# Optimization experiments

Hardware: AMD Instinct MI355X
Metric: run time of the kernel (lower is better)

## Reference

```python
import jax, jax.numpy as jnp
import numpy as np

EPS = 1e-5


def tbn(x, g, b):
    # TensorBatchNorm2d(121): normalize each of the 11x11 tensor entries over (B, C, H, W)
    mu = x.mean(axis=(0, 1, 2, 3), keepdims=True)
    var = ((x - mu) ** 2).mean(axis=(0, 1, 2, 3), keepdims=True)
    return (x - mu) * jax.lax.rsqrt(var + EPS) * g + b


def prelu(x, a):
    return jnp.where(x >= 0, x, a * x)


def tconv1x1(x, U, V):
    # x: [B,1,H,W,m,n]; U: [p,m]; V: [q,n] -> y[...,p,q] = U @ X @ V^T
    return jnp.einsum('bchwmn,pm,qn->bchwpq', x, U, V)


def tconv3x3(x, U, V):
    # x: [B,1,H,W,m,n]; U,V: [3,3,p,m] / [3,3,q,n]; pad=1, stride=1
    H, W = x.shape[2], x.shape[3]
    xp = jnp.pad(x, ((0, 0), (0, 0), (1, 1), (1, 1), (0, 0), (0, 0)))
    y = jnp.zeros(x.shape[:4] + (U.shape[2], V.shape[2]), x.dtype)
    for i in range(3):
        for j in range(3):
            y = y + jnp.einsum('bchwmn,pm,qn->bchwpq', xp[:, :, i:i + H, j:j + W], U[i, j], V[i, j])
    return y


def forward(x, f0_U, f0_V, f0_g, f0_b, f0_a, s_U, s_V, s_g, s_b,
            blk_U1, blk_V1, blk_g1, blk_b1, blk_a1,
            blk_U2, blk_V2, blk_g2, blk_b2, blk_a2,
            blk_U3, blk_V3, blk_g3, blk_b3, head_W):
    # view(-1,8,16,16,32,32).permute(0,1,4,5,2,3) -> [B,8,32,32,16,16]
    x = x.reshape(-1, 8, 16, 16, 32, 32).transpose(0, 1, 4, 5, 2, 3)
    B, H, W = x.shape[0], 32, 32
    # f0: 3x3 tensorized conv, 8 channels -> 1, tensor 16x16 -> 11x11
    xp = jnp.pad(x, ((0, 0), (0, 0), (1, 1), (1, 1), (0, 0), (0, 0)))
    y = jnp.zeros((B, H, W, 11, 11), x.dtype)
    for i in range(3):
        for j in range(3):
            y = y + jnp.einsum('bchwmn,cpm,cqn->bhwpq', xp[:, :, i:i + H, j:j + W], f0_U[:, i, j], f0_V[:, i, j])
    h = prelu(tbn(y[:, None], f0_g, f0_b), f0_a)  # [B,1,32,32,11,11]
    for k in range(4):  # four residual bottleneck blocks with 1x1 shortcut
        idn = tbn(tconv1x1(h, s_U[k], s_V[k]), s_g[k], s_b[k])
        z = prelu(tbn(tconv1x1(h, blk_U1[k], blk_V1[k]), blk_g1[k], blk_b1[k]), blk_a1[k])
        z = prelu(tbn(tconv3x3(z, blk_U2[k], blk_V2[k]), blk_g2[k], blk_b2[k]), blk_a2[k])
        z = tbn(tconv1x1(z, blk_U3[k], blk_V3[k]), blk_g3[k], blk_b3[k])
        h = z + idn
    # fcn_head: 1x1, out_type=0 -> fully contract the [11,11] tensor per class
    return jnp.einsum('bchwmn,omn->bohw', h, head_W)  # [B,21,32,32]


def setup_inputs():
    ks = jax.random.split(jax.random.key(0), 26)
    r = lambda i, s: jax.random.normal(ks[i], s, dtype=jnp.float32)
    return {
        'x': r(0, (64, 8, 16, 16, 32, 32)),
        'f0_U': r(1, (8, 3, 3, 11, 16)) * 0.1,
        'f0_V': r(2, (8, 3, 3, 11, 16)) * 0.1,
        'f0_g': r(3, (11, 11)), 'f0_b': r(4, (11, 11)),
        'f0_a': jnp.float32(0.25),
        's_U': r(5, (4, 11, 11)) * 0.3, 's_V': r(6, (4, 11, 11)) * 0.3,
        's_g': r(7, (4, 11, 11)), 's_b': r(8, (4, 11, 11)),
        'blk_U1': r(9, (4, 11, 11)) * 0.3, 'blk_V1': r(10, (4, 11, 11)) * 0.3,
        'blk_g1': r(11, (4, 11, 11)), 'blk_b1': r(12, (4, 11, 11)),
        'blk_a1': jax.random.uniform(ks[13], (4,), dtype=jnp.float32),
        'blk_U2': r(14, (4, 3, 3, 11, 11)) * 0.2, 'blk_V2': r(15, (4, 3, 3, 11, 11)) * 0.2,
        'blk_g2': r(16, (4, 11, 11)), 'blk_b2': r(17, (4, 11, 11)),
        'blk_a2': jax.random.uniform(ks[18], (4,), dtype=jnp.float32),
        'blk_U3': r(19, (4, 11, 11)) * 0.3, 'blk_V3': r(20, (4, 11, 11)) * 0.3,
        'blk_g3': r(21, (4, 11, 11)), 'blk_b3': r(22, (4, 11, 11)),
        'head_W': r(23, (21, 11, 11)) * 0.1,
    }


def reference(x, f0_U, f0_V, f0_g, f0_b, f0_a, s_U, s_V, s_g, s_b,
              blk_U1, blk_V1, blk_g1, blk_b1, blk_a1,
              blk_U2, blk_V2, blk_g2, blk_b2, blk_a2,
              blk_U3, blk_V3, blk_g3, blk_b3, head_W):
    return forward(x, f0_U, f0_V, f0_g, f0_b, f0_a, s_U, s_V, s_g, s_b,
                   blk_U1, blk_V1, blk_g1, blk_b1, blk_a1,
                   blk_U2, blk_V2, blk_g2, blk_b2, blk_a2,
                   blk_U3, blk_V3, blk_g3, blk_b3, head_W)
```

## Files before the change

### kernel.cpp

```cpp
#include <hip/hip_runtime.h>

#define NPOS 65536
#define NE   121
#define NP   6
#define NPP  4

__device__ __forceinline__ void gload_lds16(const float* g, float* l) {
  __builtin_amdgcn_global_load_lds(
      (const __attribute__((address_space(1))) void*)g,
      (__attribute__((address_space(3))) void*)l, 16, 0, 0);
}

__device__ __forceinline__ void fin_from_part(int e, const float* __restrict__ pp,
                                              const float* __restrict__ g,
                                              const float* __restrict__ bb,
                                              float& sc, float& sh) {
  float s  = pp[e * 4] + pp[e * 4 + 1] + pp[e * 4 + 2] + pp[e * 4 + 3];
  float s2 = pp[484 + e * 4] + pp[484 + e * 4 + 1] +
             pp[484 + e * 4 + 2] + pp[484 + e * 4 + 3];
  float mu  = s  * (1.f / 65536.f);
  float var = s2 * (1.f / 65536.f) - mu * mu;
  sc = g[e] * rsqrtf(var + 1e-5f);
  sh = bb[e] - mu * sc;
}

__global__ __launch_bounds__(256, 1)
void f0_kernel(const float* __restrict__ x, const float* __restrict__ U,
               const float* __restrict__ V, float* __restrict__ y,
               float* __restrict__ psum, float* __restrict__ psq) {
  __shared__ float Xb[16384];
  __shared__ float su[1152];
  __shared__ float sv[1728];

  int bid = blockIdx.x;
  int wg  = (bid & 7) * 512 + (bid >> 3);
  int ph  = wg & 1;
  int row = wg >> 1;
  int b = row >> 5, h = row & 31;
  int P0 = ph * 5;
  int t = threadIdx.x;
  int s = t >> 5, w = t & 31;

  int hlo = (h == 0) ? 0 : h - 1;
  int hhi = (h == 31) ? 31 : h + 1;
  int nh = hhi - hlo + 1;
  int nslab = 8 * nh;

  float Y[NP][11];
#pragma unroll
  for (int p = 0; p < NP; ++p)
#pragma unroll
    for (int q = 0; q < 11; ++q) Y[p][q] = 0.f;

  auto stageUV = [&](int c) {
    for (int idx = t; idx < 1152; idx += 256) {
      int tap = idx >> 7, r = idx & 127;
      int m = r >> 3, pr = r & 7;
      su[idx] = (pr < 6) ? U[(c * 9 + tap) * 176 + (P0 + pr) * 16 + m] : 0.f;
    }
    for (int idx = t; idx < 1728; idx += 256) {
      int tap = idx / 192, r = idx - tap * 192;
      int n = r / 12, q = r - n * 12;
      sv[idx] = (q < 11) ? V[(c * 9 + tap) * 176 + q * 16 + n] : 0.f;
    }
  };

  auto issueX = [&](int k) {
    int c = k / nh, hi = hlo + k % nh;
    const float* base = x + ((size_t)(b * 8 + c) << 18) + hi * 32;
    float* buf = &Xb[(k & 1) * 8192];
    int wv = t >> 6, ln = t & 63;
#pragma unroll
    for (int kk = 0; kk < 8; ++kk) {
      int chunk = wv * 8 + kk;
      int mn = chunk * 8 + (ln >> 3);
      gload_lds16(base + (size_t)mn * 1024 + (ln & 7) * 4, buf + chunk * 256);
    }
  };

  stageUV(0);
  issueX(0);

  for (int k = 0; k < nslab; ++k) {
    asm volatile("s_waitcnt vmcnt(0)" ::: "memory");
    __syncthreads();
    if (k + 1 < nslab) issueX(k + 1);

    const float* Xt = &Xb[(k & 1) * 8192];
    int c = k / nh, hi = hlo + k % nh;
    int tapbase = (hi - h + 1) * 3;
#pragma unroll
    for (int j = 0; j < 3; ++j) {
      int wj = w + j - 1;
      if ((unsigned)wj < 32u) {
        int tap = tapbase + j;
        const float* suT = &su[tap * 128];
        const float* svT = &sv[tap * 192];
        float A0[6], A1[6];
#pragma unroll
        for (int p = 0; p < 6; ++p) { A0[p] = 0.f; A1[p] = 0.f; }
#pragma unroll
        for (int m = 0; m < 16; ++m) {
          float x0 = Xt[(m * 16 + 2 * s) * 32 + wj];
          float x1 = Xt[(m * 16 + 2 * s + 1) * 32 + wj];
          float4 u0 = *(const float4*)&suT[m * 8];
          float2 u1 = *(const float2*)&suT[m * 8 + 4];
          A0[0] += u0.x * x0; A1[0] += u0.x * x1;
          A0[1] += u0.y * x0; A1[1] += u0.y * x1;
          A0[2] += u0.z * x0; A1[2] += u0.z * x1;
          A0[3] += u0.w * x0; A1[3] += u0.w * x1;
          A0[4] += u1.x * x0; A1[4] += u1.x * x1;
          A0[5] += u1.y * x0; A1[5] += u1.y * x1;
        }
#pragma unroll
        for (int nn = 0; nn < 2; ++nn) {
          const float* vb = &svT[(2 * s + nn) * 12];
          float4 v0 = *(const float4*)&vb[0];
          float4 v1 = *(const float4*)&vb[4];
          float4 v2 = *(const float4*)&vb[8];
          float vq[11] = { v0.x, v0.y, v0.z, v0.w,
                           v1.x, v1.y, v1.z, v1.w,
                           v2.x, v2.y, v2.z };
          const float* Ax = nn ? A1 : A0;
#pragma unroll
          for (int p = 0; p < 6; ++p)
#pragma unroll
            for (int q = 0; q < 11; ++q)
              Y[p][q] += Ax[p] * vq[q];
        }
      }
    }
    if (k + 1 < nslab && (k % nh) == nh - 1) {
      __syncthreads();
      stageUV(c + 1);
    }
  }

  int posb = ((b << 5) + h) << 5;
#pragma unroll
  for (int p = 0; p < NP; ++p) {
    __syncthreads();
#pragma unroll
    for (int q = 0; q < 11; ++q) Xb[t * 11 + q] = Y[p][q];
    __syncthreads();
    for (int rep = 0; rep < 2; ++rep) {
      int idx = rep * 256 + t;
      if (idx < 352) {
        int qq = idx >> 5, w2 = idx & 31;
        float v = 0.f;
#pragma unroll
        for (int s2 = 0; s2 < 8; ++s2) v += Xb[(s2 * 32 + w2) * 11 + qq];
        int e = (P0 + p) * 11 + qq;
        y[(size_t)e * NPOS + posb + w2] = v;
        float sm = v, sq = v * v;
#pragma unroll
        for (int d = 16; d > 0; d >>= 1) {
          sm += __shfl_down(sm, d, 32);
          sq += __shfl_down(sq, d, 32);
        }
        if (w2 == 0) {
          psum[(size_t)e * 2048 + row] = sm;
          psq [(size_t)e * 2048 + row] = sq;
        }
      }
    }
  }
}

__global__ __launch_bounds__(256)
void f0_stats_final(const float* __restrict__ psum, const float* __restrict__ psq,
                    const float* __restrict__ g, const float* __restrict__ bb,
                    float* __restrict__ sc, float* __restrict__ sh) {
  int e = blockIdx.x, t = threadIdx.x;
  float s = 0.f, s2 = 0.f;
  for (int i = t; i < 2048; i += 256) {
    s  += psum[(size_t)e * 2048 + i];
    s2 += psq [(size_t)e * 2048 + i];
  }
#pragma unroll
  for (int o = 32; o > 0; o >>= 1) {
    s  += __shfl_down(s, o);
    s2 += __shfl_down(s2, o);
  }
  __shared__ float ls[8];
  int wid = t >> 6;
  if ((t & 63) == 0) { ls[wid] = s; ls[4 + wid] = s2; }
  __syncthreads();
  if (t == 0) {
    float ss  = ls[0] + ls[1] + ls[2] + ls[3];
    float ss2 = ls[4] + ls[5] + ls[6] + ls[7];
    float mu  = ss  * (1.f / 65536.f);
    float var = ss2 * (1.f / 65536.f) - mu * mu;
    float sca = g[e] * rsqrtf(var + 1e-5f);
    sc[e] = sca;
    sh[e] = bb[e] - mu * sca;
  }
}

__global__ __launch_bounds__(256)
void stats_partial(const float* __restrict__ raw, float* __restrict__ part) {
  int blk = blockIdx.x;
  int e = blk >> 2, qt = blk & 3;
  const float4* p = (const float4*)(raw + (size_t)e * NPOS) + qt * 4096;
  int t = threadIdx.x;
  float s = 0.f, s2 = 0.f;
  for (int i = t; i < 4096; i += 256) {
    float4 v = p[i];
    s  += v.x + v.y + v.z + v.w;
    s2 += v.x * v.x + v.y * v.y + v.z * v.z + v.w * v.w;
  }
#pragma unroll
  for (int o = 32; o > 0; o >>= 1) {
    s  += __shfl_down(s, o);
    s2 += __shfl_down(s2, o);
  }
  __shared__ float ls[8];
  int wid = t >> 6;
  if ((t & 63) == 0) { ls[wid] = s; ls[4 + wid] = s2; }
  __syncthreads();
  if (t == 0) {
    part[blk]       = ls[0] + ls[1] + ls[2] + ls[3];
    part[484 + blk] = ls[4] + ls[5] + ls[6] + ls[7];
  }
}

__global__ __launch_bounds__(256)
void stats_partial_dual(const float* __restrict__ rawA, float* __restrict__ partA,
                        const float* __restrict__ rawB, float* __restrict__ partB) {
  int blk = blockIdx.x;
  int sel = blk >= 484;
  int lblk = sel ? blk - 484 : blk;
  const float* raw = sel ? rawB : rawA;
  float* part = sel ? partB : partA;
  int e = lblk >> 2, qt = lblk & 3;
  const float4* p = (const float4*)(raw + (size_t)e * NPOS) + qt * 4096;
  int t = threadIdx.x;
  float s = 0.f, s2 = 0.f;
  for (int i = t; i < 4096; i += 256) {
    float4 v = p[i];
    s  += v.x + v.y + v.z + v.w;
    s2 += v.x * v.x + v.y * v.y + v.z * v.z + v.w * v.w;
  }
#pragma unroll
  for (int o = 32; o > 0; o >>= 1) {
    s  += __shfl_down(s, o);
    s2 += __shfl_down(s2, o);
  }
  __shared__ float ls[8];
  int wid = t >> 6;
  if ((t & 63) == 0) { ls[wid] = s; ls[4 + wid] = s2; }
  __syncthreads();
  if (t == 0) {
    part[lblk]       = ls[0] + ls[1] + ls[2] + ls[3];
    part[484 + lblk] = ls[4] + ls[5] + ls[6] + ls[7];
  }
}

template<bool HASB, bool PRELU, bool FINA, bool FINB>
__global__ __launch_bounds__(256, 2)
void conv1x1_dual(const float* __restrict__ rA,
                  const float* __restrict__ scA, const float* __restrict__ shA,
                  const float* __restrict__ pA, const float* __restrict__ gA,
                  const float* __restrict__ bA,
                  const float* __restrict__ rB,
                  const float* __restrict__ pB, const float* __restrict__ gB,
                  const float* __restrict__ bB,
                  const float* __restrict__ alpha_ptr, int alpha_idx,
                  const float* __restrict__ U1, const float* __restrict__ V1,
                  float* __restrict__ out1,
                  const float* __restrict__ U2, const float* __restrict__ V2,
                  float* __restrict__ out2) {
  __shared__ float su1[NPP * 11], su2[NPP * 11], sv1[121], sv2[121];
  __shared__ float sa[242], sb[242];
  int bid = blockIdx.x;
  int wg  = (bid & 7) * 96 + (bid >> 3);
  int part = wg % 3, posblk = wg / 3;
  int P0 = part * 4;
  int pmax = (part == 2) ? 3 : 4;
  int t = threadIdx.x;
  if (t < 121) {
    sv1[t] = V1[t]; sv2[t] = V2[t];
    if (FINA) fin_from_part(t, pA, gA, bA, sa[t], sb[t]);
    else      { sa[t] = scA[t]; sb[t] = shA[t]; }
    if (HASB) {
      if (FINB) fin_from_part(t, pB, gB, bB, sa[121 + t], sb[121 + t]);
    }
  }
  if (t < NPP * 11) {
    int pr = t / 11, mm = t - pr * 11;
    int srow = P0 + pr; if (srow > 10) srow = 10;
    su1[t] = U1[srow * 11 + mm];
    su2[t] = U2[srow * 11 + mm];
  }
  __syncthreads();
  float alpha = 0.f;
  if (PRELU) alpha = alpha_ptr[alpha_idx];
  size_t pos = (size_t)posblk * 256 + t;

  float T1[NPP][11], T2[NPP][11];
#pragma unroll
  for (int p = 0; p < NPP; ++p)
#pragma unroll
    for (int n = 0; n < 11; ++n) { T1[p][n] = 0.f; T2[p][n] = 0.f; }

#pragma unroll 2
  for (int m = 0; m < 11; ++m) {
    float Xr[11];
#pragma unroll
    for (int n = 0; n < 11; ++n) {
      int e = m * 11 + n;
      float v = sa[e] * rA[(size_t)e * NPOS + pos] + sb[e];
      if (HASB) v += sa[121 + e] * rB[(size_t)e * NPOS + pos] + sb[121 + e];
      if (PRELU) v = v >= 0.f ? v : alpha * v;
      Xr[n] = v;
    }
#pragma unroll
    for (int p = 0; p < NPP; ++p) {
      float u1 = su1[p * 11 + m];
      float u2 = su2[p * 11 + m];
#pragma unroll
      for (int n = 0; n < 11; ++n) {
        T1[p][n] += u1 * Xr[n];
        T2[p][n] += u2 * Xr[n];
      }
    }
  }
#pragma unroll
  for (int q = 0; q < 11; ++q) {
    float Yc1[NPP], Yc2[NPP];
#pragma unroll
    for (int p = 0; p < NPP; ++p) { Yc1[p] = 0.f; Yc2[p] = 0.f; }
#pragma unroll
    for (int n = 0; n < 11; ++n) {
      float v1 = sv1[q * 11 + n];
      float v2 = sv2[q * 11 + n];
#pragma unroll
      for (int p = 0; p < NPP; ++p) {
        Yc1[p] += T1[p][n] * v1;
        Yc2[p] += T2[p][n] * v2;
      }
    }
    for (int p = 0; p < pmax; ++p) {
      out1[(size_t)((P0 + p) * 11 + q) * NPOS + pos] = Yc1[p];
      out2[(size_t)((P0 + p) * 11 + q) * NPOS + pos] = Yc2[p];
    }
  }
}

template<bool PRELU>
__global__ __launch_bounds__(256, 2)
void conv1x1_kernel(const float* __restrict__ rA,
                    const float* __restrict__ pA, const float* __restrict__ gA,
                    const float* __restrict__ bA,
                    const float* __restrict__ alpha_ptr, int alpha_idx,
                    const float* __restrict__ U, const float* __restrict__ V,
                    float* __restrict__ out) {
  __shared__ float su[NP * 11], sv[121], sa[242], sb[242];
  int bid = blockIdx.x;
  int wg  = (bid & 7) * 64 + (bid >> 3);
  int ph = wg & 1, posblk = wg >> 1;
  int P0 = ph * 5;
  int t = threadIdx.x;
  if (t < 121) {
    sv[t] = V[t];
    fin_from_part(t, pA, gA, bA, sa[t], sb[t]);
  }
  if (t < NP * 11) su[t] = U[P0 * 11 + t];
  __syncthreads();
  float alpha = 0.f;
  if (PRELU) alpha = alpha_ptr[alpha_idx];
  size_t pos = (size_t)posblk * 256 + t;

  float T[NP][11];
#pragma unroll
  for (int p = 0; p < NP; ++p)
#pragma unroll
    for (int n = 0; n < 11; ++n) T[p][n] = 0.f;

#pragma unroll 2
  for (int m = 0; m < 11; ++m) {
    float Xr[11];
#pragma unroll
    for (int n = 0; n < 11; ++n) {
      int e = m * 11 + n;
      float v = sa[e] * rA[(size_t)e * NPOS + pos] + sb[e];
      if (PRELU) v = v >= 0.f ? v : alpha * v;
      Xr[n] = v;
    }
#pragma unroll
    for (int p = 0; p < NP; ++p) {
      float u = su[p * 11 + m];
#pragma unroll
      for (int n = 0; n < 11; ++n) T[p][n] += u * Xr[n];
    }
  }
#pragma unroll
  for (int q = 0; q < 11; ++q) {
    float Yc[NP];
#pragma unroll
    for (int p = 0; p < NP; ++p) Yc[p] = 0.f;
#pragma unroll
    for (int n = 0; n < 11; ++n) {
      float v = sv[q * 11 + n];
#pragma unroll
      for (int p = 0; p < NP; ++p) Yc[p] += T[p][n] * v;
    }
#pragma unroll
    for (int p = 0; p < NP; ++p)
      out[(size_t)((P0 + p) * 11 + q) * NPOS + pos] = Yc[p];
  }
}

template<int N0, int NW>
__device__ __forceinline__ void c3_chunk(const float* __restrict__ rA,
    const float* __restrict__ sa, const float* __restrict__ sh,
    const float* __restrict__ su, const float* __restrict__ sv,
    float alpha, int npos, float (&Y)[NP][11]) {
  float T[NP][NW];
#pragma unroll
  for (int p = 0; p < NP; ++p)
#pragma unroll
    for (int k = 0; k < NW; ++k) T[p][k] = 0.f;
#pragma unroll 2
  for (int m = 0; m < 11; ++m) {
    float Xr[NW];
#pragma unroll
    for (int k = 0; k < NW; ++k) {
      int e = m * 11 + N0 + k;
      float v = sa[e] * rA[(size_t)e * NPOS + npos] + sh[e];
      Xr[k] = v >= 0.f ? v : alpha * v;
    }
#pragma unroll
    for (int p = 0; p < NP; ++p) {
      float u = su[p * 11 + m];
#pragma unroll
      for (int k = 0; k < NW; ++k) T[p][k] += u * Xr[k];
    }
  }
#pragma unroll
  for (int k = 0; k < NW; ++k) {
#pragma unroll
    for (int q = 0; q < 11; ++q) {
      float v = sv[q * 11 + N0 + k];
#pragma unroll
      for (int p = 0; p < NP; ++p) Y[p][q] += T[p][k] * v;
    }
  }
}

__global__ __launch_bounds__(256, 2)
void conv3x3_kernel(const float* __restrict__ rA,
                    const float* __restrict__ pA, const float* __restrict__ gA,
                    const float* __restrict__ bA,
                    const float* __restrict__ alpha_ptr, int alpha_idx,
                    const float* __restrict__ U, const float* __restrict__ V,
                    float* __restrict__ out) {
  __shared__ float su[9 * NP * 11], sv[1089], sa[121], sh[121];
  int bid = blockIdx.x;
  int wg  = (bid & 7) * 64 + (bid >> 3);
  int ph = wg & 1, posblk = wg >> 1;
  int P0 = ph * 5;
  int t = threadIdx.x;
  for (int idx = t; idx < 9 * NP * 11; idx += 256) {
    int ij = idx / (NP * 11), r = idx - ij * (NP * 11);
    su[idx] = U[ij * 121 + P0 * 11 + r];
  }
  for (int idx = t; idx < 1089; idx += 256) sv[idx] = V[idx];
  if (t < 121) fin_from_part(t, pA, gA, bA, sa[t], sh[t]);
  __syncthreads();
  float alpha = alpha_ptr[alpha_idx];
  int pos = posblk * 256 + t;
  int b = pos >> 10, h = (pos >> 5) & 31, w = pos & 31;

  float Y[NP][11];
#pragma unroll
  for (int p = 0; p < NP; ++p)
#pragma unroll
    for (int q = 0; q < 11; ++q) Y[p][q] = 0.f;

  for (int ij = 0; ij < 9; ++ij) {
    int i = ij / 3, j = ij - 3 * (ij / 3);
    int hi = h + i - 1, wj = w + j - 1;
    if ((unsigned)hi >= 32u || (unsigned)wj >= 32u) continue;
    int npos = ((b << 5) + hi) * 32 + wj;
    const float* suij = &su[ij * NP * 11];
    const float* svij = &sv[ij * 121];
    c3_chunk<0, 4>(rA, sa, sh, suij, svij, alpha, npos, Y);
    c3_chunk<4, 4>(rA, sa, sh, suij, svij, alpha, npos, Y);
    c3_chunk<8, 3>(rA, sa, sh, suij, svij, alpha, npos, Y);
  }
#pragma unroll
  for (int p = 0; p < NP; ++p)
#pragma unroll
    for (int q = 0; q < 11; ++q)
      out[(size_t)((P0 + p) * 11 + q) * NPOS + pos] = Y[p][q];
}

__global__ __launch_bounds__(256, 2)
void head_kernel(const float* __restrict__ rA,
                 const float* __restrict__ pA, const float* __restrict__ gA,
                 const float* __restrict__ bA,
                 const float* __restrict__ rB,
                 const float* __restrict__ pB, const float* __restrict__ gB,
                 const float* __restrict__ bB,
                 const float* __restrict__ W, float* __restrict__ out) {
  __shared__ float sw[21 * 121], sa[242], sh[242];
  int t = threadIdx.x;
  for (int idx = t; idx < 2541; idx += 256) sw[idx] = W[idx];
  if (t < 121) {
    fin_from_part(t, pA, gA, bA, sa[t], sh[t]);
    fin_from_part(t, pB, gB, bB, sa[121 + t], sh[121 + t]);
  }
  __syncthreads();
  size_t pos = (size_t)blockIdx.x * 256 + t;
  int b = (int)(pos >> 10), hw = (int)(pos & 1023);
  float acc[21];
#pragma unroll
  for (int o = 0; o < 21; ++o) acc[o] = 0.f;
  for (int e = 0; e < 121; ++e) {
    float v = sa[e] * rA[(size_t)e * NPOS + pos] + sh[e] +
              sa[121 + e] * rB[(size_t)e * NPOS + pos] + sh[121 + e];
#pragma unroll
    for (int o = 0; o < 21; ++o) acc[o] += v * sw[o * 121 + e];
  }
#pragma unroll
  for (int o = 0; o < 21; ++o)
    out[(size_t)(b * 21 + o) * 1024 + hw] = acc[o];
}

extern "C" void kernel_launch(void* const* d_in, const int* in_sizes, int n_in,
                              void* d_out, int out_size, void* d_ws, size_t ws_size,
                              hipStream_t stream) {
  (void)in_sizes; (void)n_in; (void)out_size; (void)ws_size;
  const float* x     = (const float*)d_in[0];
  const float* f0_U  = (const float*)d_in[1];
  const float* f0_V  = (const float*)d_in[2];
  const float* f0_g  = (const float*)d_in[3];
  const float* f0_b  = (const float*)d_in[4];
  const float* f0_a  = (const float*)d_in[5];
  const float* s_U   = (const float*)d_in[6];
  const float* s_V   = (const float*)d_in[7];
  const float* s_g   = (const float*)d_in[8];
  const float* s_b   = (const float*)d_in[9];
  const float* bU1   = (const float*)d_in[10];
  const float* bV1   = (const float*)d_in[11];
  const float* bg1   = (const float*)d_in[12];
  const float* bb1   = (const float*)d_in[13];
  const float* ba1   = (const float*)d_in[14];
  const float* bU2   = (const float*)d_in[15];
  const float* bV2   = (const float*)d_in[16];
  const float* bg2   = (const float*)d_in[17];
  const float* bb2   = (const float*)d_in[18];
  const float* ba2   = (const float*)d_in[19];
  const float* bU3   = (const float*)d_in[20];
  const float* bV3   = (const float*)d_in[21];
  const float* bg3   = (const float*)d_in[22];
  const float* bb3   = (const float*)d_in[23];
  const float* headW = (const float*)d_in[24];

  float* ws = (float*)d_ws;
  const size_t BUF = (size_t)NE * NPOS;
  float* B[4]  = { ws, ws + BUF, ws + 2 * BUF, ws + 3 * BUF };
  float* st    = ws + 4 * BUF;
  float* psum  = st + 242;
  float* psq   = psum + 121 * 2048;
  float* pb0   = psq + 121 * 2048;
  float* pb1   = pb0 + 968;
  float* pb2   = pb1 + 968;
  float* pb3   = pb2 + 968;

  f0_kernel<<<4096, 256, 0, stream>>>(x, f0_U, f0_V, B[0], psum, psq);
  f0_stats_final<<<121, 256, 0, stream>>>(psum, psq, f0_g, f0_b, st, st + 121);

  const int bufs[4][4] = { {1,2,3,0}, {2,3,0,1}, {3,0,1,2}, {0,1,2,3} };

  const float* hA = B[0];
  const float* hB = nullptr;

  for (int k = 0; k < 4; ++k) {
    float* idn = B[bufs[k][0]];
    float* z1  = B[bufs[k][1]];
    float* z2  = B[bufs[k][2]];
    float* z3  = B[bufs[k][3]];

    if (k == 0) {
      conv1x1_dual<false, true, false, false><<<768, 256, 0, stream>>>(
          hA, st, st + 121, nullptr, nullptr, nullptr,
          nullptr, nullptr, nullptr, nullptr,
          f0_a, 0,
          s_U + k * 121, s_V + k * 121, idn,
          bU1 + k * 121, bV1 + k * 121, z1);
    } else {
      conv1x1_dual<true, false, true, true><<<768, 256, 0, stream>>>(
          hA, nullptr, nullptr, pb3, bg3 + (k - 1) * 121, bb3 + (k - 1) * 121,
          hB, pb0, s_g + (k - 1) * 121, s_b + (k - 1) * 121,
          nullptr, 0,
          s_U + k * 121, s_V + k * 121, idn,
          bU1 + k * 121, bV1 + k * 121, z1);
    }
    stats_partial_dual<<<968, 256, 0, stream>>>(idn, pb0, z1, pb1);

    conv3x3_kernel<<<512, 256, 0, stream>>>(
        z1, pb1, bg1 + k * 121, bb1 + k * 121, ba1, k,
        bU2 + k * 1089, bV2 + k * 1089, z2);
    stats_partial<<<484, 256, 0, stream>>>(z2, pb2);

    conv1x1_kernel<true><<<512, 256, 0, stream>>>(
        z2, pb2, bg2 + k * 121, bb2 + k * 121, ba2, k,
        bU3 + k * 121, bV3 + k * 121, z3);
    stats_partial<<<484, 256, 0, stream>>>(z3, pb3);

    hA = z3;
    hB = idn;
  }

  head_kernel<<<256, 256, 0, stream>>>(
      hA, pb3, bg3 + 3 * 121, bb3 + 3 * 121,
      hB, pb0, s_g + 3 * 121, s_b + 3 * 121,
      headW, (float*)d_out);
}
```

Measured before the change: 1.640 ms.

## Split f0 input slab into two m-halves to halve LDS staging buffer

The f0 kernel now streams each (channel, row) slab as two halves over the m index, double-buffering 4096-float chunks instead of 8192. Partial U-contractions for all three column taps are kept in registers across the two halves, and the V contraction into Y runs only after the second half. This halves the shared-memory footprint, which could allow more resident blocks or finer-grained load/compute overlap. The costs are twice as many barriers and loop iterations plus 36 extra accumulator registers, under launch_bounds(256,1).

```diff
diff --git a/kernel.cpp b/kernel.cpp
--- a/kernel.cpp
+++ b/kernel.cpp
@@ -28,7 +28,7 @@
 void f0_kernel(const float* __restrict__ x, const float* __restrict__ U,
                const float* __restrict__ V, float* __restrict__ y,
                float* __restrict__ psum, float* __restrict__ psq) {
-  __shared__ float Xb[16384];
+  __shared__ float Xb[8192];
   __shared__ float su[1152];
   __shared__ float sv[1728];
 
@@ -44,13 +44,19 @@
   int hlo = (h == 0) ? 0 : h - 1;
   int hhi = (h == 31) ? 31 : h + 1;
   int nh = hhi - hlo + 1;
-  int nslab = 8 * nh;
+  int nslab = 8 * nh * 2;
 
   float Y[NP][11];
 #pragma unroll
   for (int p = 0; p < NP; ++p)
 #pragma unroll
     for (int q = 0; q < 11; ++q) Y[p][q] = 0.f;
+
+  float A[3][NP][2];
+#pragma unroll
+  for (int j = 0; j < 3; ++j)
+#pragma unroll
+    for (int p = 0; p < NP; ++p) { A[j][p][0] = 0.f; A[j][p][1] = 0.f; }
 
   auto stageUV = [&](int c) {
     for (int idx = t; idx < 1152; idx += 256) {
@@ -66,15 +72,17 @@
   };
 
   auto issueX = [&](int k) {
-    int c = k / nh, hi = hlo + k % nh;
+    int c = k / (2 * nh), rem = k % (2 * nh);
+    int hi = hlo + (rem >> 1), half = rem & 1;
     const float* base = x + ((size_t)(b * 8 + c) << 18) + hi * 32;
-    float* buf = &Xb[(k & 1) * 8192];
+    float* buf = &Xb[(k & 1) * 4096];
     int wv = t >> 6, ln = t & 63;
 #pragma unroll
-    for (int kk = 0; kk < 8; ++kk) {
-      int chunk = wv * 8 + kk;
+    for (int kk = 0; kk < 4; ++kk) {
+      int chunk = wv * 4 + kk;
       int mn = chunk * 8 + (ln >> 3);
-      gload_lds16(base + (size_t)mn * 1024 + (ln & 7) * 4, buf + chunk * 256);
+      gload_lds16(base + (size_t)(half * 128 + mn) * 1024 + (ln & 7) * 4,
+                  buf + chunk * 256);
     }
   };
 
@@ -86,53 +94,64 @@
     __syncthreads();
     if (k + 1 < nslab) issueX(k + 1);
 
-    const float* Xt = &Xb[(k & 1) * 8192];
-    int c = k / nh, hi = hlo + k % nh;
+    const float* Xt = &Xb[(k & 1) * 4096];
+    int rem = k % (2 * nh);
+    int hi = hlo + (rem >> 1), half = rem & 1;
     int tapbase = (hi - h + 1) * 3;
+    int mbase = half * 8;
+
 #pragma unroll
     for (int j = 0; j < 3; ++j) {
       int wj = w + j - 1;
       if ((unsigned)wj < 32u) {
+        const float* suT = &su[(tapbase + j) * 128 + mbase * 8];
+#pragma unroll
+        for (int mm = 0; mm < 8; ++mm) {
+          float x0 = Xt[(mm * 16 + 2 * s) * 32 + wj];
+          float x1 = Xt[(mm * 16 + 2 * s + 1) * 32 + wj];
+          float4 u0 = *(const float4*)&suT[mm * 8];
+          float2 u1 = *(const float2*)&suT[mm * 8 + 4];
+          A[j][0][0] += u0.x * x0; A[j][0][1] += u0.x * x1;
+          A[j][1][0] += u0.y * x0; A[j][1][1] += u0.y * x1;
+          A[j][2][0] += u0.z * x0; A[j][2][1] += u0.z * x1;
+          A[j][3][0] += u0.w * x0; A[j][3][1] += u0.w * x1;
+          A[j][4][0] += u1.x * x0; A[j][4][1] += u1.x * x1;
+          A[j][5][0] += u1.y * x0; A[j][5][1] += u1.y * x1;
+        }
+      }
+    }
+
+    if (half == 1) {
+#pragma unroll
+      for (int j = 0; j < 3; ++j) {
         int tap = tapbase + j;
-        const float* suT = &su[tap * 128];
-        const float* svT = &sv[tap * 192];
-        float A0[6], A1[6];
-#pragma unroll
-        for (int p = 0; p < 6; ++p) { A0[p] = 0.f; A1[p] = 0.f; }
-#pragma unroll
-        for (int m = 0; m < 16; ++m) {
-          float x0 = Xt[(m * 16 + 2 * s) * 32 + wj];
-          float x1 = Xt[(m * 16 + 2 * s + 1) * 32 + wj];
-          float4 u0 = *(const float4*)&suT[m * 8];
-          float2 u1 = *(const float2*)&suT[m * 8 + 4];
-          A0[0] += u0.x * x0; A1[0] += u0.x * x1;
-          A0[1] += u0.y * x0; A1[1] += u0.y * x1;
-          A0[2] += u0.z * x0; A1[2] += u0.z * x1;
-          A0[3] += u0.w * x0; A1[3] += u0.w * x1;
-          A0[4] += u1.x * x0; A1[4] += u1.x * x1;
-          A0[5] += u1.y * x0; A1[5] += u1.y * x1;
-        }
 #pragma unroll
         for (int nn = 0; nn < 2; ++nn) {
-          const float* vb = &svT[(2 * s + nn) * 12];
+          const float* vb = &sv[tap * 192 + (2 * s + nn) * 12];
           float4 v0 = *(const float4*)&vb[0];
           float4 v1 = *(const float4*)&vb[4];
           float4 v2 = *(const float4*)&vb[8];
           float vq[11] = { v0.x, v0.y, v0.z, v0.w,
                            v1.x, v1.y, v1.z, v1.w,
                            v2.x, v2.y, v2.z };
-          const float* Ax = nn ? A1 : A0;
-#pragma unroll
-          for (int p = 0; p < 6; ++p)
+#pragma unroll
+          for (int p = 0; p < NP; ++p) {
+            float a = A[j][p][nn];
 #pragma unroll
             for (int q = 0; q < 11; ++q)
-              Y[p][q] += Ax[p] * vq[q];
+              Y[p][q] += a * vq[q];
+          }
         }
       }
-    }
-    if (k + 1 < nslab && (k % nh) == nh - 1) {
+#pragma unroll
+      for (int j = 0; j < 3; ++j)
+#pragma unroll
+        for (int p = 0; p < NP; ++p) { A[j][p][0] = 0.f; A[j][p][1] = 0.f; }
+    }
+
+    if (k + 1 < nslab && rem == 2 * nh - 1) {
       __syncthreads();
-      stageUV(c + 1);
+      stageUV(k / (2 * nh) + 1);
     }
   }
 
```

New measurement: 1.754 ms. 1.07x slower.
